# Optimization experiments

Measured on AMD Instinct MI355X. Metric: run time of the kernel, lower is better.

## Reference

```python
import jax, jax.numpy as jnp
import numpy as np


def _lstm_scan(x, mask, W_ih, W_hh, h0, c0):
    # x: [B,S,D], mask: [B,S] bool. Masked LSTM (bias=False, PyTorch gate order i,f,g,o).
    def step(carry, inp):
        h, c = carry
        xt, mt = inp
        gates = xt @ W_ih.T + h @ W_hh.T          # [B, 4H]
        i, f, g, o = jnp.split(gates, 4, axis=-1)
        c_new = jax.nn.sigmoid(f) * c + jax.nn.sigmoid(i) * jnp.tanh(g)
        h_new = jax.nn.sigmoid(o) * jnp.tanh(c_new)
        m = mt[:, None]
        h = jnp.where(m, h_new, h)
        c = jnp.where(m, c_new, c)
        return (h, c), h
    (hT, cT), hs = jax.lax.scan(step, (h0, c0), (x.swapaxes(0, 1), mask.T))
    return hs.swapaxes(0, 1), hT, cT  # [B,S,H], [B,H], [B,H]


def setup_inputs() -> dict:
    key = jax.random.key(0)
    ks = jax.random.split(key, 24)
    B, S, V, E, H, DA, R, MH = 64, 1024, 50000, 300, 256, 64, 16, 512
    N_ET, N_PRT, N_POPT = 50, 12, 8
    sc = 1.0 / np.sqrt(H)
    input_ids = jax.random.randint(ks[0], (B, S), 0, V)
    len_li = jnp.sort(jax.random.randint(ks[1], (B,), S // 2, S + 1))[::-1]  # descending, >=1
    inp = {
        'input_ids': input_ids,
        'len_li': len_li,
        'h0': jnp.zeros((2, B, H), jnp.float32),
        'c0': jnp.zeros((2, B, H), jnp.float32),
        'emb': jax.random.normal(ks[2], (V, E), jnp.float32) * 0.1,
        'W_ih_f': jax.random.normal(ks[3], (4 * H, E), jnp.float32) * sc,
        'W_hh_f': jax.random.normal(ks[4], (4 * H, H), jnp.float32) * sc,
        'W_ih_b': jax.random.normal(ks[5], (4 * H, E), jnp.float32) * sc,
        'W_hh_b': jax.random.normal(ks[6], (4 * H, H), jnp.float32) * sc,
        'S1': jax.random.uniform(ks[7], (DA, 2 * H), jnp.float32, -0.1, 0.1),
        'S2': jax.random.uniform(ks[8], (R, DA), jnp.float32, -0.1, 0.1),
        'W_et': jax.random.uniform(ks[9], (MH, R * 2 * H), jnp.float32, -0.1, 0.1),
        'b_et': jnp.zeros((MH,), jnp.float32),
        'Wd_et': jax.random.uniform(ks[10], (N_ET, MH), jnp.float32, -0.1, 0.1),
        'bd_et': jnp.zeros((N_ET,), jnp.float32),
        'W_prt': jax.random.uniform(ks[11], (MH, R * 2 * H), jnp.float32, -0.1, 0.1),
        'b_prt': jnp.zeros((MH,), jnp.float32),
        'Wd_prt': jax.random.uniform(ks[12], (N_PRT, MH), jnp.float32, -0.1, 0.1),
        'bd_prt': jnp.zeros((N_PRT,), jnp.float32),
        'W_popt': jax.random.uniform(ks[13], (MH, R * 2 * H), jnp.float32, -0.1, 0.1),
        'b_popt': jnp.zeros((MH,), jnp.float32),
        'Wd_popt': jax.random.uniform(ks[14], (N_POPT, MH), jnp.float32, -0.1, 0.1),
        'bd_popt': jnp.zeros((N_POPT,), jnp.float32),
    }
    return inp


def reference(input_ids, len_li, h0, c0, emb, W_ih_f, W_hh_f, W_ih_b, W_hh_b,
              S1, S2, W_et, b_et, Wd_et, bd_et, W_prt, b_prt, Wd_prt, bd_prt,
              W_popt, b_popt, Wd_popt, bd_popt):
    B, S = input_ids.shape
    t = jnp.arange(S)[None, :]
    mask = t < len_li[:, None]                                  # [B,S]
    x = emb[input_ids]                                          # [B,S,E]
    # forward direction
    out_f, hf, cf = _lstm_scan(x, mask, W_ih_f, W_hh_f, h0[0], c0[0])
    # backward direction: reverse each sequence within its own length (involution)
    rev_idx = jnp.clip(len_li[:, None] - 1 - t, 0, S - 1)       # [B,S]
    x_rev = jnp.take_along_axis(x, rev_idx[:, :, None], axis=1)
    out_b_rev, hb, cb = _lstm_scan(x_rev, mask, W_ih_b, W_hh_b, h0[1], c0[1])
    out_b = jnp.take_along_axis(out_b_rev, rev_idx[:, :, None], axis=1)
    Hout = jnp.concatenate([out_f, out_b], axis=-1)             # [B,S,2H]
    # self-attention: A = softmax over valid positions, per row of r
    s2 = jnp.tanh(Hout @ S1.T) @ S2.T                           # [B,S,r]
    NEG = jnp.asarray(-1e30, Hout.dtype)
    scores = jnp.where(mask[:, :, None], s2, NEG).swapaxes(1, 2)  # [B,r,S]
    A = jax.nn.softmax(scores, axis=-1)                         # [B,r,S]
    M = jnp.einsum('brs,bsd->brd', A, Hout)                     # [B,r,2H]
    BM = M.reshape(B, -1)                                       # [B, r*2H]
    AAT = jnp.einsum('brs,bqs->brq', A, A)                      # [B,r,r]
    I = jnp.eye(A.shape[1], dtype=A.dtype)
    penal = jnp.mean(jnp.sum((AAT - I) ** 2, axis=(1, 2)))      # mean ||AA^T - I||_F^2
    def head(W, b, Wd, bd):
        return jax.nn.relu(BM @ W.T + b) @ Wd.T + bd
    decoded_et = head(W_et, b_et, Wd_et, bd_et)
    decoded_prt = head(W_prt, b_prt, Wd_prt, bd_prt)
    decoded_popt = head(W_popt, b_popt, Wd_popt, bd_popt)
    hidden = (jnp.stack([hf, hb]), jnp.stack([cf, cb]))
    return (decoded_et, decoded_prt, decoded_popt, hidden, penal, A)
```

## Files before the change

kernel.cpp:

```cpp
#include <hip/hip_runtime.h>
#include <cstdint>
#include <cstddef>

typedef short bf16x8 __attribute__((ext_vector_type(8)));
typedef float f32x4 __attribute__((ext_vector_type(4)));

#define DEVI static __device__ __forceinline__

DEVI unsigned short f2bf(float f) {
  union { float f; unsigned u; } v; v.f = f;
  unsigned r = (v.u + 0x7fffu + ((v.u >> 16) & 1u)) >> 16;
  return (unsigned short)r;
}
DEVI float bf2f(unsigned short s) {
  union { unsigned u; float f; } v; v.u = ((unsigned)s) << 16;
  return v.f;
}
DEVI float sigf(float x) { return 1.f / (1.f + __expf(-x)); }
DEVI float tanh_f(float x) {
  float xc = fminf(fmaxf(x, -15.f), 15.f);
  float e = __expf(2.f * xc);
  return 1.f - 2.f / (e + 1.f);
}
DEVI unsigned long long ldg_sc1_64(const unsigned long long* p) {
  return __hip_atomic_load(p, __ATOMIC_RELAXED, __HIP_MEMORY_SCOPE_AGENT);
}
DEVI void stg_sc1(unsigned* p, unsigned v) {
  __hip_atomic_store(p, v, __ATOMIC_RELAXED, __HIP_MEMORY_SCOPE_AGENT);
}

#define DO_ET     0
#define DO_PRT    3200
#define DO_POPT   3968
#define DO_H      4480
#define DO_C      37248
#define DO_PENAL  70016
#define DO_A      70017

__global__ __launch_bounds__(256) void k_pack(
    const float* __restrict__ Wih_f, const float* __restrict__ Wih_b,
    const float* __restrict__ Whh_f, const float* __restrict__ Whh_b,
    const float* __restrict__ S1,
    unsigned short* __restrict__ BihP, unsigned short* __restrict__ BhhP,
    unsigned short* __restrict__ S1P, int* __restrict__ flags, float* __restrict__ dout)
{
  int idx = blockIdx.x * 256 + threadIdx.x;
  if (idx < 655360) {
    int d = idx / 327680; int e = idx % 327680;
    int kb = e / 8192; int rem = e % 8192; int n = rem >> 3; int j = rem & 7;
    int k = kb * 8 + j;
    int col = ((n >> 5) & 3) * 256 + ((n >> 7) << 5) + (n & 31);
    const float* W = d ? Wih_b : Wih_f;
    float v = (k < 300) ? W[col * 300 + k] : 0.f;
    BihP[idx] = f2bf(v);
  } else if (idx < 1179648) {
    int e = idx - 655360;
    int d = e >> 18; int e2 = e & 262143;
    int ht = (e2 >> 15) & 7; int kb = (e2 >> 10) & 31; int c = (e2 >> 3) & 127; int j = e2 & 7;
    int k = kb * 8 + j;
    int row = ((c >> 5) << 8) + (ht << 5) + (c & 31);
    const float* W = d ? Whh_b : Whh_f;
    BhhP[e] = f2bf(W[row * 256 + k]);
  } else if (idx < 1212416) {
    int e = idx - 1179648;
    int j = e & 7; int da = (e >> 3) & 63; int kb = e >> 9;
    S1P[e] = f2bf(S1[da * 512 + kb * 8 + j]);
  } else if (idx < 1213440) {
    flags[idx - 1212416] = 0;
  } else if (idx == 1213440) {
    dout[DO_PENAL] = 0.f;
  }
}

__global__ __launch_bounds__(256, 1) void k_rnn(
    const int* __restrict__ ids, const float* __restrict__ emb,
    const unsigned short* __restrict__ BihP, const unsigned short* __restrict__ BhhP,
    unsigned short* __restrict__ Hbuf, unsigned short* __restrict__ Hout, int* flags,
    const int* __restrict__ len, const float* __restrict__ h0, const float* __restrict__ c0,
    float* __restrict__ dout)
{
  int blk = blockIdx.x;
  int ht = blk >> 3; int g = blk & 7; int d = g >> 2; int bt = g & 3;
  int tid = threadIdx.x;
  int lane = tid & 63, w = tid >> 6, l15 = lane & 15, quad = lane >> 4;
  int b0 = bt * 16;

  __shared__ unsigned short Wl[40960];
  __shared__ unsigned short Xl[2][5120];
  __shared__ unsigned short h0p[4096];
  __shared__ float gatesL[2048];
  __shared__ int lenS[16];

  {
    const unsigned* src = (const unsigned*)(BihP + (size_t)d * 327680);
    unsigned* dstW = (unsigned*)Wl;
    for (int kb = 0; kb < 40; ++kb) {
      int gb = ((kb * 1024 + ht * 128) * 8) >> 1;
      for (int i = tid; i < 512; i += 256)
        dstW[kb * 512 + i] = src[gb + i];
    }
  }
  for (int i = tid; i < 4096; i += 256) {
    int kb = i >> 7, mm = (i >> 3) & 15, j = i & 7;
    h0p[i] = f2bf(h0[d * 16384 + (b0 + mm) * 256 + kb * 8 + j]);
  }
  if (tid < 16) lenS[tid] = len[b0 + tid];
  for (int i = tid; i < 128; i += 256) {
    ((unsigned*)Xl[0])[2432 + i] = 0;
    ((unsigned*)Xl[1])[2432 + i] = 0;
  }
  const unsigned short* Bw = BhhP + (size_t)(d * 8 + ht) * 32768;
  bf16x8 bfr[8][2];
  #pragma unroll
  for (int kc = 0; kc < 8; ++kc)
    #pragma unroll
    for (int nt = 0; nt < 2; ++nt)
      bfr[kc][nt] = *reinterpret_cast<const bf16x8*>(
          Bw + ((size_t)(kc * 4 + quad) * 128 + w * 32 + nt * 16 + l15) * 8);

  __syncthreads();

  int xm = tid >> 4, xf = tid & 15;
  {
    int lbm = lenS[xm];
    int s = d ? (lbm - 1) : 0;
    s = s < 0 ? 0 : (s > 1023 ? 1023 : s);
    int tok = ids[(b0 + xm) * 1024 + s];
    const float* er = emb + (size_t)tok * 300;
    #pragma unroll
    for (int i = 0; i < 5; ++i) {
      int f = xf + 16 * i;
      float4 v = (f <= 74) ? *reinterpret_cast<const float4*>(er + 4 * f)
                           : (float4){0.f, 0.f, 0.f, 0.f};
      if (f < 76) {
        int uo = ((f >> 1) * 16 + xm) * 4 + (f & 1) * 2;
        ((unsigned*)Xl[0])[uo]     = (unsigned)f2bf(v.x) | ((unsigned)f2bf(v.y) << 16);
        ((unsigned*)Xl[0])[uo + 1] = (unsigned)f2bf(v.z) | ((unsigned)f2bf(v.w) << 16);
      }
    }
  }
  __syncthreads();

  int b_l = tid >> 4, u2 = tid & 15;
  int len_b = lenS[b_l];
  int Tmax = lenS[0];
  int cidx = d * 16384 + (b0 + b_l) * 256 + ht * 32 + 2 * u2;
  float cc0 = c0[cidx], cc1 = c0[cidx + 1];
  float hh0 = h0[cidx], hh1 = h0[cidx + 1];

  unsigned short* HbufG = Hbuf + (size_t)g * 8192;
  int* fl = flags + g * 128;

  for (int t = 0; t < Tmax; ++t) {
    float4 xr[5];
    {
      int tn = t + 1;
      int s = d ? (lenS[xm] - 1 - tn) : tn;
      s = s < 0 ? 0 : (s > 1023 ? 1023 : s);
      int tok = ids[(b0 + xm) * 1024 + s];
      const float* er = emb + (size_t)tok * 300;
      #pragma unroll
      for (int i = 0; i < 5; ++i) {
        int f = xf + 16 * i;
        xr[i] = (f <= 74) ? *reinterpret_cast<const float4*>(er + 4 * f)
                          : (float4){0.f, 0.f, 0.f, 0.f};
      }
    }

    f32x4 ac0 = {0.f, 0.f, 0.f, 0.f}, ac1 = {0.f, 0.f, 0.f, 0.f};
    {
      const unsigned short* Xb = Xl[t & 1];
      #pragma unroll
      for (int kc = 0; kc < 10; ++kc) {
        int kb = kc * 4 + quad;
        bf16x8 ax  = *reinterpret_cast<const bf16x8*>(&Xb[(kb * 16 + l15) * 8]);
        bf16x8 bx0 = *reinterpret_cast<const bf16x8*>(&Wl[kb * 1024 + (w * 32 + l15) * 8]);
        bf16x8 bx1 = *reinterpret_cast<const bf16x8*>(&Wl[kb * 1024 + (w * 32 + 16 + l15) * 8]);
        ac0 = __builtin_amdgcn_mfma_f32_16x16x32_bf16(ax, bx0, ac0, 0, 0, 0);
        ac1 = __builtin_amdgcn_mfma_f32_16x16x32_bf16(ax, bx1, ac1, 0, 0, 0);
      }
    }

    bf16x8 ah[8];
    if (t == 0) {
      #pragma unroll
      for (int kc = 0; kc < 8; ++kc)
        ah[kc] = *reinterpret_cast<const bf16x8*>(&h0p[((kc * 4 + quad) * 16 + l15) * 8]);
    } else {
      int polls = 0;
      while (true) {
        int v = 0x7fffffff;
        if (lane < 8)
          v = __hip_atomic_load(fl + lane * 16, __ATOMIC_RELAXED, __HIP_MEMORY_SCOPE_AGENT);
        if (__ballot(v >= t) == ~0ull) break;
        if (++polls > 100000) break;
      }
      asm volatile("" ::: "memory");
      const unsigned long long* slotU =
          (const unsigned long long*)(HbufG + (size_t)(t & 1) * 4096);
      #pragma unroll
      for (int kc = 0; kc < 8; ++kc) {
        int qo = (((kc * 4 + quad) * 16 + l15) * 4) >> 1;
        union { unsigned long long q[2]; bf16x8 v; } tu;
        tu.q[0] = ldg_sc1_64(slotU + qo);
        tu.q[1] = ldg_sc1_64(slotU + qo + 1);
        ah[kc] = tu.v;
      }
    }
    #pragma unroll
    for (int kc = 0; kc < 8; ++kc) {
      ac0 = __builtin_amdgcn_mfma_f32_16x16x32_bf16(ah[kc], bfr[kc][0], ac0, 0, 0, 0);
      ac1 = __builtin_amdgcn_mfma_f32_16x16x32_bf16(ah[kc], bfr[kc][1], ac1, 0, 0, 0);
    }

    #pragma unroll
    for (int r = 0; r < 4; ++r) {
      gatesL[(w * 16 + quad * 4 + r) * 32 + l15] = ac0[r];
      gatesL[(w * 16 + quad * 4 + r) * 32 + 16 + l15] = ac1[r];
    }
    __syncthreads();

    float gi0 = gatesL[(0 * 16 + b_l) * 32 + 2 * u2], gi1 = gatesL[(0 * 16 + b_l) * 32 + 2 * u2 + 1];
    float gf0 = gatesL[(1 * 16 + b_l) * 32 + 2 * u2], gf1 = gatesL[(1 * 16 + b_l) * 32 + 2 * u2 + 1];
    float gg0 = gatesL[(2 * 16 + b_l) * 32 + 2 * u2], gg1 = gatesL[(2 * 16 + b_l) * 32 + 2 * u2 + 1];
    float go0 = gatesL[(3 * 16 + b_l) * 32 + 2 * u2], go1 = gatesL[(3 * 16 + b_l) * 32 + 2 * u2 + 1];

    if (t < len_b) {
      float cn0 = sigf(gf0) * cc0 + sigf(gi0) * tanh_f(gg0);
      float cn1 = sigf(gf1) * cc1 + sigf(gi1) * tanh_f(gg1);
      cc0 = cn0; cc1 = cn1;
      hh0 = sigf(go0) * tanh_f(cn0);
      hh1 = sigf(go1) * tanh_f(cn1);
    }

    int k = ht * 32 + 2 * u2;
    unsigned hp = (unsigned)f2bf(hh0) | ((unsigned)f2bf(hh1) << 16);
    unsigned soff = ((unsigned)(k >> 3) * 128 + b_l * 8 + (k & 7)) >> 1;
    stg_sc1((unsigned*)(HbufG + (size_t)((t + 1) & 1) * 4096) + soff, hp);

    {
      unsigned* LX = (unsigned*)Xl[(t + 1) & 1];
      #pragma unroll
      for (int i = 0; i < 5; ++i) {
        int f = xf + 16 * i;
        if (f < 76) {
          int uo = ((f >> 1) * 16 + xm) * 4 + (f & 1) * 2;
          LX[uo]     = (unsigned)f2bf(xr[i].x) | ((unsigned)f2bf(xr[i].y) << 16);
          LX[uo + 1] = (unsigned)f2bf(xr[i].z) | ((unsigned)f2bf(xr[i].w) << 16);
        }
      }
    }

    __syncthreads();
    if (tid == 0)
      __hip_atomic_store(fl + ht * 16, t + 1, __ATOMIC_RELAXED, __HIP_MEMORY_SCOPE_AGENT);

    size_t hob = (size_t)(b0 + b_l) * 524288;
    if (d == 0) {
      *reinterpret_cast<unsigned*>(Hout + hob + (size_t)t * 512 + k) = hp;
    } else if (t < len_b) {
      *reinterpret_cast<unsigned*>(Hout + hob + (size_t)(len_b - 1 - t) * 512 + 256 + k) = hp;
    }
    if (t == len_b - 1) {
      dout[DO_H + cidx] = hh0; dout[DO_H + cidx + 1] = hh1;
      dout[DO_C + cidx] = cc0; dout[DO_C + cidx + 1] = cc1;
    }
  }
}

__global__ __launch_bounds__(256, 2) void k_scores(
    const unsigned short* __restrict__ Hout, const unsigned short* __restrict__ S1P,
    const float* __restrict__ S2, float* __restrict__ scores)
{
  __shared__ float U[128 * 65];
  __shared__ float S2l[16 * 65];
  int tid = threadIdx.x;
  int t0 = blockIdx.x * 128;
  int b = blockIdx.y;
  int lane = tid & 63, w = tid >> 6, l15 = lane & 15, quad = lane >> 4;

  f32x4 acc[2][4];
  #pragma unroll
  for (int i = 0; i < 2; ++i)
    #pragma unroll
    for (int j = 0; j < 4; ++j) acc[i][j] = (f32x4){0.f, 0.f, 0.f, 0.f};

  for (int kc = 0; kc < 16; ++kc) {
    bf16x8 afr[2];
    #pragma unroll
    for (int mt = 0; mt < 2; ++mt) {
      int row = t0 + w * 32 + mt * 16 + l15;
      afr[mt] = *reinterpret_cast<const bf16x8*>(
          Hout + (size_t)b * 524288 + (size_t)row * 512 + kc * 32 + quad * 8);
    }
    bf16x8 bfr[4];
    #pragma unroll
    for (int nt = 0; nt < 4; ++nt)
      bfr[nt] = *reinterpret_cast<const bf16x8*>(
          S1P + ((size_t)(kc * 4 + quad) * 64 + nt * 16 + l15) * 8);
    #pragma unroll
    for (int mt = 0; mt < 2; ++mt)
      #pragma unroll
      for (int nt = 0; nt < 4; ++nt)
        acc[mt][nt] = __builtin_amdgcn_mfma_f32_16x16x32_bf16(afr[mt], bfr[nt], acc[mt][nt], 0, 0, 0);
  }
  #pragma unroll
  for (int mt = 0; mt < 2; ++mt)
    #pragma unroll
    for (int nt = 0; nt < 4; ++nt)
      #pragma unroll
      for (int r = 0; r < 4; ++r)
        U[(w * 32 + mt * 16 + quad * 4 + r) * 65 + nt * 16 + l15] = acc[mt][nt][r];
  for (int i = tid; i < 1024; i += 256) S2l[(i >> 6) * 65 + (i & 63)] = S2[i];
  __syncthreads();
  for (int i = tid; i < 8192; i += 256) {
    int row = i >> 6, c = i & 63;
    U[row * 65 + c] = tanh_f(U[row * 65 + c]);
  }
  __syncthreads();
  for (int idx = tid; idx < 2048; idx += 256) {
    int row = idx >> 4, r = idx & 15;
    float s = 0.f;
    #pragma unroll 8
    for (int da = 0; da < 64; ++da) s += U[row * 65 + da] * S2l[r * 65 + da];
    scores[((size_t)b * 16 + r) * 1024 + t0 + row] = s;
  }
}

__global__ __launch_bounds__(256) void k_softmax(
    const float* __restrict__ scores, const int* __restrict__ len, float* __restrict__ dout)
{
  __shared__ float red[256];
  int b = blockIdx.x, r = blockIdx.y;
  int tid = threadIdx.x;
  int lb = len[b];
  const float* src = scores + ((size_t)b * 16 + r) * 1024;
  float v[4]; float mx = -3.0e38f;
  #pragma unroll
  for (int i = 0; i < 4; ++i) {
    int t = tid + i * 256;
    v[i] = (t < lb) ? src[t] : -3.0e38f;
    mx = fmaxf(mx, v[i]);
  }
  red[tid] = mx; __syncthreads();
  for (int s = 128; s > 0; s >>= 1) { if (tid < s) red[tid] = fmaxf(red[tid], red[tid + s]); __syncthreads(); }
  float M = red[0]; __syncthreads();
  float se = 0.f;
  #pragma unroll
  for (int i = 0; i < 4; ++i) {
    int t = tid + i * 256;
    if (t < lb) { v[i] = __expf(v[i] - M); se += v[i]; }
  }
  red[tid] = se; __syncthreads();
  for (int s = 128; s > 0; s >>= 1) { if (tid < s) red[tid] += red[tid + s]; __syncthreads(); }
  float inv = 1.f / red[0];
  float* dst = dout + DO_A + ((size_t)b * 16 + r) * 1024;
  #pragma unroll
  for (int i = 0; i < 4; ++i) {
    int t = tid + i * 256;
    dst[t] = (t < lb) ? v[i] * inv : 0.f;
  }
}

__global__ __launch_bounds__(256) void k_penal(float* __restrict__ dout)
{
  __shared__ float Al[16 * 513];
  __shared__ float red[256];
  int b = blockIdx.x, tid = threadIdx.x;
  const float* A = dout + DO_A + (size_t)b * 16384;
  int r = tid >> 4, q = tid & 15;
  float s = 0.f;
  for (int half = 0; half < 2; ++half) {
    __syncthreads();
    for (int i = tid; i < 8192; i += 256) {
      int rr = i >> 9, t = i & 511;
      Al[rr * 513 + t] = A[rr * 1024 + half * 512 + t];
    }
    __syncthreads();
    for (int t = 0; t < 512; ++t) s += Al[r * 513 + t] * Al[q * 513 + t];
  }
  float dv = s - ((r == q) ? 1.f : 0.f);
  red[tid] = dv * dv; __syncthreads();
  for (int st = 128; st > 0; st >>= 1) { if (tid < st) red[tid] += red[tid + st]; __syncthreads(); }
  if (tid == 0) atomicAdd(dout + DO_PENAL, red[0] * (1.f / 64.f));
}

__global__ __launch_bounds__(256) void k_attnM(
    const float* __restrict__ dout, const unsigned short* __restrict__ Hout,
    const int* __restrict__ len, float* __restrict__ Mws)
{
  int b = blockIdx.x, dc = blockIdx.y;
  int tid = threadIdx.x;
  int col = dc * 128 + (tid & 127);
  int rh = tid >> 7;
  int lb = len[b];
  const float* Ab = dout + DO_A + (size_t)b * 16384;
  const unsigned short* Hb = Hout + (size_t)b * 524288;
  float acc[8];
  #pragma unroll
  for (int i = 0; i < 8; ++i) acc[i] = 0.f;
  for (int t = 0; t < lb; ++t) {
    float h = bf2f(Hb[(size_t)t * 512 + col]);
    #pragma unroll
    for (int rr = 0; rr < 8; ++rr) acc[rr] += Ab[(rh * 8 + rr) * 1024 + t] * h;
  }
  #pragma unroll
  for (int rr = 0; rr < 8; ++rr) Mws[(size_t)b * 8192 + (rh * 8 + rr) * 512 + col] = acc[rr];
}

__global__ __launch_bounds__(256) void k_heads1(
    const float* __restrict__ W, const float* __restrict__ Mws, float* __restrict__ P)
{
  int tid = threadIdx.x;
  int n = blockIdx.x * 16 + (tid & 15);
  int ks = blockIdx.y;
  int bg = tid >> 4;
  const float* Wr = W + (size_t)n * 8192 + ks * 1024;
  float acc[4] = {0.f, 0.f, 0.f, 0.f};
  for (int k = 0; k < 1024; k += 4) {
    float4 wv = *reinterpret_cast<const float4*>(Wr + k);
    #pragma unroll
    for (int i = 0; i < 4; ++i) {
      float4 mv = *reinterpret_cast<const float4*>(Mws + (size_t)(bg * 4 + i) * 8192 + ks * 1024 + k);
      acc[i] += wv.x * mv.x + wv.y * mv.y + wv.z * mv.z + wv.w * mv.w;
    }
  }
  #pragma unroll
  for (int i = 0; i < 4; ++i)
    P[(size_t)(ks * 64 + bg * 4 + i) * 512 + n] = acc[i];
}

__global__ __launch_bounds__(256) void k_headred(
    const float* __restrict__ Pws, const float* __restrict__ b_et,
    const float* __restrict__ b_prt, const float* __restrict__ b_popt,
    float* __restrict__ hid)
{
  int idx = blockIdx.x * 256 + threadIdx.x;
  int head = idx >> 15; int rem = idx & 32767;
  int b = rem >> 9; int n = rem & 511;
  const float* bias = (head == 0) ? b_et : (head == 1) ? b_prt : b_popt;
  float s = bias[n];
  #pragma unroll
  for (int ks = 0; ks < 8; ++ks)
    s += Pws[(size_t)(head * 8 + ks) * 32768 + b * 512 + n];
  hid[idx] = fmaxf(s, 0.f);
}

__global__ __launch_bounds__(256) void k_head2(
    const float* __restrict__ hid, const float* __restrict__ Wd, const float* __restrict__ bd,
    float* __restrict__ out, int No)
{
  int idx = blockIdx.x * 256 + threadIdx.x;
  if (idx >= 64 * No) return;
  int b = idx / No, o = idx % No;
  const float* hv = hid + (size_t)b * 512;
  const float* wr = Wd + (size_t)o * 512;
  float acc = bd[o];
  for (int k = 0; k < 512; k += 4) {
    float4 h4 = *reinterpret_cast<const float4*>(hv + k);
    float4 w4 = *reinterpret_cast<const float4*>(wr + k);
    acc += h4.x * w4.x + h4.y * w4.y + h4.z * w4.z + h4.w * w4.w;
  }
  out[idx] = acc;
}

extern "C" void kernel_launch(void* const* d_in, const int* in_sizes, int n_in,
                              void* d_out, int out_size, void* d_ws, size_t ws_size,
                              hipStream_t stream) {
  const int*   ids    = (const int*)d_in[0];
  const int*   len    = (const int*)d_in[1];
  const float* h0     = (const float*)d_in[2];
  const float* c0     = (const float*)d_in[3];
  const float* emb    = (const float*)d_in[4];
  const float* Wih_f  = (const float*)d_in[5];
  const float* Whh_f  = (const float*)d_in[6];
  const float* Wih_b  = (const float*)d_in[7];
  const float* Whh_b  = (const float*)d_in[8];
  const float* S1     = (const float*)d_in[9];
  const float* S2     = (const float*)d_in[10];
  const float* W_et   = (const float*)d_in[11];
  const float* b_et   = (const float*)d_in[12];
  const float* Wd_et  = (const float*)d_in[13];
  const float* bd_et  = (const float*)d_in[14];
  const float* W_prt  = (const float*)d_in[15];
  const float* b_prt  = (const float*)d_in[16];
  const float* Wd_prt = (const float*)d_in[17];
  const float* bd_prt = (const float*)d_in[18];
  const float* W_popt = (const float*)d_in[19];
  const float* b_popt = (const float*)d_in[20];
  const float* Wd_popt= (const float*)d_in[21];
  const float* bd_popt= (const float*)d_in[22];
  float* dout = (float*)d_out;
  char* ws = (char*)d_ws;

  size_t off = 0;
  auto AL = [&](size_t bytes) { size_t r = off; off += (bytes + 255) & ~(size_t)255; return r; };
  size_t oHout = AL(67108864UL);
  size_t oBih  = AL(1310720UL);
  size_t oBhh  = AL(1048576UL);
  size_t oS1P  = AL(65536UL);
  size_t oHbuf = AL(131072UL);
  size_t oFlag = AL(4096UL);
  size_t oPws  = AL(3145728UL);
  size_t oSc   = AL(4194304UL);
  size_t oM    = oSc;
  size_t oHid  = oSc + 2097152UL;

  unsigned short* Hout = (unsigned short*)(ws + oHout);
  unsigned short* BihP = (unsigned short*)(ws + oBih);
  unsigned short* BhhP = (unsigned short*)(ws + oBhh);
  unsigned short* S1P  = (unsigned short*)(ws + oS1P);
  unsigned short* Hbuf = (unsigned short*)(ws + oHbuf);
  int* flags           = (int*)(ws + oFlag);
  float* Pws           = (float*)(ws + oPws);
  float* scores        = (float*)(ws + oSc);
  float* Mws           = (float*)(ws + oM);
  float* hid           = (float*)(ws + oHid);

  hipLaunchKernelGGL(k_pack, dim3(4741), dim3(256), 0, stream,
                     Wih_f, Wih_b, Whh_f, Whh_b, S1, BihP, BhhP, S1P, flags, dout);
  hipLaunchKernelGGL(k_rnn, dim3(64), dim3(256), 0, stream,
                     ids, emb, BihP, BhhP, Hbuf, Hout, flags, len, h0, c0, dout);
  hipLaunchKernelGGL(k_scores, dim3(8, 64), dim3(256), 0, stream, Hout, S1P, S2, scores);
  hipLaunchKernelGGL(k_softmax, dim3(64, 16), dim3(256), 0, stream, scores, len, dout);
  hipLaunchKernelGGL(k_penal, dim3(64), dim3(256), 0, stream, dout);
  hipLaunchKernelGGL(k_attnM, dim3(64, 4), dim3(256), 0, stream, dout, Hout, len, Mws);
  hipLaunchKernelGGL(k_heads1, dim3(32, 8), dim3(256), 0, stream, W_et,   Mws, Pws);
  hipLaunchKernelGGL(k_heads1, dim3(32, 8), dim3(256), 0, stream, W_prt,  Mws, Pws + 262144);
  hipLaunchKernelGGL(k_heads1, dim3(32, 8), dim3(256), 0, stream, W_popt, Mws, Pws + 524288);
  hipLaunchKernelGGL(k_headred, dim3(384), dim3(256), 0, stream, Pws, b_et, b_prt, b_popt, hid);
  hipLaunchKernelGGL(k_head2, dim3(13), dim3(256), 0, stream, hid,         Wd_et,   bd_et,   dout + DO_ET, 50);
  hipLaunchKernelGGL(k_head2, dim3(3),  dim3(256), 0, stream, hid + 32768, Wd_prt,  bd_prt,  dout + DO_PRT, 12);
  hipLaunchKernelGGL(k_head2, dim3(2),  dim3(256), 0, stream, hid + 65536, Wd_popt, bd_popt, dout + DO_POPT, 8);
}
```

Baseline: 3.456 ms.

## Keep all LSTM weights in registers and split hidden dim over 4 blocks

```diff
diff --git a/kernel.cpp b/kernel.cpp
--- a/kernel.cpp
+++ b/kernel.cpp
@@ -25,7 +25,7 @@
 DEVI unsigned long long ldg_sc1_64(const unsigned long long* p) {
   return __hip_atomic_load(p, __ATOMIC_RELAXED, __HIP_MEMORY_SCOPE_AGENT);
 }
-DEVI void stg_sc1(unsigned* p, unsigned v) {
+DEVI void stg_sc1_64(unsigned long long* p, unsigned long long v) {
   __hip_atomic_store(p, v, __ATOMIC_RELAXED, __HIP_MEMORY_SCOPE_AGENT);
 }
 
@@ -46,21 +46,29 @@
 {
   int idx = blockIdx.x * 256 + threadIdx.x;
   if (idx < 655360) {
-    int d = idx / 327680; int e = idx % 327680;
-    int kb = e / 8192; int rem = e % 8192; int n = rem >> 3; int j = rem & 7;
-    int k = kb * 8 + j;
-    int col = ((n >> 5) & 3) * 256 + ((n >> 7) << 5) + (n & 31);
+    int dq = idx / 81920; int e = idx % 81920;
+    int d = dq >> 2; int q = dq & 3;
+    int j = e & 7; int lane = (e >> 3) & 63;
+    int r1 = e >> 9;
+    int kc = r1 % 10; int wg = r1 / 10;
+    int gg = wg & 3; int w = wg >> 2;
+    int l15 = lane & 15, quad = lane >> 4;
+    int row = gg * 256 + q * 64 + w * 16 + l15;
+    int k = kc * 32 + quad * 8 + j;
     const float* W = d ? Wih_b : Wih_f;
-    float v = (k < 300) ? W[col * 300 + k] : 0.f;
+    float v = (k < 300) ? W[row * 300 + k] : 0.f;
     BihP[idx] = f2bf(v);
   } else if (idx < 1179648) {
-    int e = idx - 655360;
-    int d = e >> 18; int e2 = e & 262143;
-    int ht = (e2 >> 15) & 7; int kb = (e2 >> 10) & 31; int c = (e2 >> 3) & 127; int j = e2 & 7;
-    int k = kb * 8 + j;
-    int row = ((c >> 5) << 8) + (ht << 5) + (c & 31);
+    int e0 = idx - 655360;
+    int dq = e0 >> 16; int e = e0 & 65535;
+    int d = dq >> 2; int q = dq & 3;
+    int j = e & 7; int lane = (e >> 3) & 63;
+    int kc = (e >> 9) & 7; int gg = (e >> 12) & 3; int w = e >> 14;
+    int l15 = lane & 15, quad = lane >> 4;
+    int row = gg * 256 + q * 64 + w * 16 + l15;
+    int k = kc * 32 + quad * 8 + j;
     const float* W = d ? Whh_b : Whh_f;
-    BhhP[e] = f2bf(W[row * 256 + k]);
+    BhhP[e0] = f2bf(W[row * 256 + k]);
   } else if (idx < 1212416) {
     int e = idx - 1179648;
     int j = e & 7; int da = (e >> 3) & 63; int kb = e >> 9;
@@ -80,26 +88,32 @@
     float* __restrict__ dout)
 {
   int blk = blockIdx.x;
-  int ht = blk >> 3; int g = blk & 7; int d = g >> 2; int bt = g & 3;
+  int q = blk >> 3;
+  int g = blk & 7; int d = g >> 2; int bt = g & 3;
   int tid = threadIdx.x;
   int lane = tid & 63, w = tid >> 6, l15 = lane & 15, quad = lane >> 4;
   int b0 = bt * 16;
 
-  __shared__ unsigned short Wl[40960];
   __shared__ unsigned short Xl[2][5120];
   __shared__ unsigned short h0p[4096];
-  __shared__ float gatesL[2048];
   __shared__ int lenS[16];
 
-  {
-    const unsigned* src = (const unsigned*)(BihP + (size_t)d * 327680);
-    unsigned* dstW = (unsigned*)Wl;
-    for (int kb = 0; kb < 40; ++kb) {
-      int gb = ((kb * 1024 + ht * 128) * 8) >> 1;
-      for (int i = tid; i < 512; i += 256)
-        dstW[kb * 512 + i] = src[gb + i];
-    }
-  }
+  const unsigned short* BA = BihP + (size_t)(d * 4 + q) * 81920;
+  const unsigned short* BH = BhhP + (size_t)(d * 4 + q) * 65536;
+  bf16x8 wih[4][10];
+  bf16x8 whh[4][8];
+  #pragma unroll
+  for (int gg = 0; gg < 4; ++gg) {
+    #pragma unroll
+    for (int kc = 0; kc < 10; ++kc)
+      wih[gg][kc] = *reinterpret_cast<const bf16x8*>(
+          BA + ((size_t)(((w * 4 + gg) * 10 + kc) * 64 + lane)) * 8);
+    #pragma unroll
+    for (int kc = 0; kc < 8; ++kc)
+      whh[gg][kc] = *reinterpret_cast<const bf16x8*>(
+          BH + ((size_t)(((w * 4 + gg) * 8 + kc) * 64 + lane)) * 8);
+  }
+
   for (int i = tid; i < 4096; i += 256) {
     int kb = i >> 7, mm = (i >> 3) & 15, j = i & 7;
     h0p[i] = f2bf(h0[d * 16384 + (b0 + mm) * 256 + kb * 8 + j]);
@@ -109,21 +123,12 @@
     ((unsigned*)Xl[0])[2432 + i] = 0;
     ((unsigned*)Xl[1])[2432 + i] = 0;
   }
-  const unsigned short* Bw = BhhP + (size_t)(d * 8 + ht) * 32768;
-  bf16x8 bfr[8][2];
-  #pragma unroll
-  for (int kc = 0; kc < 8; ++kc)
-    #pragma unroll
-    for (int nt = 0; nt < 2; ++nt)
-      bfr[kc][nt] = *reinterpret_cast<const bf16x8*>(
-          Bw + ((size_t)(kc * 4 + quad) * 128 + w * 32 + nt * 16 + l15) * 8);
-
   __syncthreads();
 
   int xm = tid >> 4, xf = tid & 15;
+  int len_xm = lenS[xm];
   {
-    int lbm = lenS[xm];
-    int s = d ? (lbm - 1) : 0;
+    int s = d ? (len_xm - 1) : 0;
     s = s < 0 ? 0 : (s > 1023 ? 1023 : s);
     int tok = ids[(b0 + xm) * 1024 + s];
     const float* er = emb + (size_t)tok * 300;
@@ -141,21 +146,28 @@
   }
   __syncthreads();
 
-  int b_l = tid >> 4, u2 = tid & 15;
-  int len_b = lenS[b_l];
+  int len_my = lenS[l15];
   int Tmax = lenS[0];
-  int cidx = d * 16384 + (b0 + b_l) * 256 + ht * 32 + 2 * u2;
-  float cc0 = c0[cidx], cc1 = c0[cidx + 1];
-  float hh0 = h0[cidx], hh1 = h0[cidx + 1];
+  int dimb = q * 64 + w * 16 + quad * 4;
+  int cidx = d * 16384 + (b0 + l15) * 256 + dimb;
+  float cc[4], hh[4];
+  {
+    float4 c4 = *reinterpret_cast<const float4*>(c0 + cidx);
+    float4 h4 = *reinterpret_cast<const float4*>(h0 + cidx);
+    cc[0] = c4.x; cc[1] = c4.y; cc[2] = c4.z; cc[3] = c4.w;
+    hh[0] = h4.x; hh[1] = h4.y; hh[2] = h4.z; hh[3] = h4.w;
+  }
 
   unsigned short* HbufG = Hbuf + (size_t)g * 8192;
   int* fl = flags + g * 128;
+  int slotKB = dimb >> 3;
+  int slotJ  = dimb & 7;
 
   for (int t = 0; t < Tmax; ++t) {
     float4 xr[5];
     {
       int tn = t + 1;
-      int s = d ? (lenS[xm] - 1 - tn) : tn;
+      int s = d ? (len_xm - 1 - tn) : tn;
       s = s < 0 ? 0 : (s > 1023 ? 1023 : s);
       int tok = ids[(b0 + xm) * 1024 + s];
       const float* er = emb + (size_t)tok * 300;
@@ -167,17 +179,17 @@
       }
     }
 
-    f32x4 ac0 = {0.f, 0.f, 0.f, 0.f}, ac1 = {0.f, 0.f, 0.f, 0.f};
+    f32x4 acc0 = {0.f, 0.f, 0.f, 0.f};
+    f32x4 acc1 = acc0, acc2 = acc0, acc3 = acc0;
     {
       const unsigned short* Xb = Xl[t & 1];
       #pragma unroll
       for (int kc = 0; kc < 10; ++kc) {
-        int kb = kc * 4 + quad;
-        bf16x8 ax  = *reinterpret_cast<const bf16x8*>(&Xb[(kb * 16 + l15) * 8]);
-        bf16x8 bx0 = *reinterpret_cast<const bf16x8*>(&Wl[kb * 1024 + (w * 32 + l15) * 8]);
-        bf16x8 bx1 = *reinterpret_cast<const bf16x8*>(&Wl[kb * 1024 + (w * 32 + 16 + l15) * 8]);
-        ac0 = __builtin_amdgcn_mfma_f32_16x16x32_bf16(ax, bx0, ac0, 0, 0, 0);
-        ac1 = __builtin_amdgcn_mfma_f32_16x16x32_bf16(ax, bx1, ac1, 0, 0, 0);
+        bf16x8 bx = *reinterpret_cast<const bf16x8*>(&Xb[((kc * 4 + quad) * 16 + l15) * 8]);
+        acc0 = __builtin_amdgcn_mfma_f32_16x16x32_bf16(wih[0][kc], bx, acc0, 0, 0, 0);
+        acc1 = __builtin_amdgcn_mfma_f32_16x16x32_bf16(wih[1][kc], bx, acc1, 0, 0, 0);
+        acc2 = __builtin_amdgcn_mfma_f32_16x16x32_bf16(wih[2][kc], bx, acc2, 0, 0, 0);
+        acc3 = __builtin_amdgcn_mfma_f32_16x16x32_bf16(wih[3][kc], bx, acc3, 0, 0, 0);
       }
     }
 
@@ -190,7 +202,7 @@
       int polls = 0;
       while (true) {
         int v = 0x7fffffff;
-        if (lane < 8)
+        if (lane < 4)
           v = __hip_atomic_load(fl + lane * 16, __ATOMIC_RELAXED, __HIP_MEMORY_SCOPE_AGENT);
         if (__ballot(v >= t) == ~0ull) break;
         if (++polls > 100000) break;
@@ -200,43 +212,52 @@
           (const unsigned long long*)(HbufG + (size_t)(t & 1) * 4096);
       #pragma unroll
       for (int kc = 0; kc < 8; ++kc) {
-        int qo = (((kc * 4 + quad) * 16 + l15) * 4) >> 1;
-        union { unsigned long long q[2]; bf16x8 v; } tu;
-        tu.q[0] = ldg_sc1_64(slotU + qo);
-        tu.q[1] = ldg_sc1_64(slotU + qo + 1);
+        int qo = ((kc * 4 + quad) * 16 + l15) * 2;
+        union { unsigned long long u[2]; bf16x8 v; } tu;
+        tu.u[0] = ldg_sc1_64(slotU + qo);
+        tu.u[1] = ldg_sc1_64(slotU + qo + 1);
         ah[kc] = tu.v;
       }
     }
     #pragma unroll
     for (int kc = 0; kc < 8; ++kc) {
-      ac0 = __builtin_amdgcn_mfma_f32_16x16x32_bf16(ah[kc], bfr[kc][0], ac0, 0, 0, 0);
-      ac1 = __builtin_amdgcn_mfma_f32_16x16x32_bf16(ah[kc], bfr[kc][1], ac1, 0, 0, 0);
-    }
-
-    #pragma unroll
-    for (int r = 0; r < 4; ++r) {
-      gatesL[(w * 16 + quad * 4 + r) * 32 + l15] = ac0[r];
-      gatesL[(w * 16 + quad * 4 + r) * 32 + 16 + l15] = ac1[r];
-    }
-    __syncthreads();
-
-    float gi0 = gatesL[(0 * 16 + b_l) * 32 + 2 * u2], gi1 = gatesL[(0 * 16 + b_l) * 32 + 2 * u2 + 1];
-    float gf0 = gatesL[(1 * 16 + b_l) * 32 + 2 * u2], gf1 = gatesL[(1 * 16 + b_l) * 32 + 2 * u2 + 1];
-    float gg0 = gatesL[(2 * 16 + b_l) * 32 + 2 * u2], gg1 = gatesL[(2 * 16 + b_l) * 32 + 2 * u2 + 1];
-    float go0 = gatesL[(3 * 16 + b_l) * 32 + 2 * u2], go1 = gatesL[(3 * 16 + b_l) * 32 + 2 * u2 + 1];
-
-    if (t < len_b) {
-      float cn0 = sigf(gf0) * cc0 + sigf(gi0) * tanh_f(gg0);
-      float cn1 = sigf(gf1) * cc1 + sigf(gi1) * tanh_f(gg1);
-      cc0 = cn0; cc1 = cn1;
-      hh0 = sigf(go0) * tanh_f(cn0);
-      hh1 = sigf(go1) * tanh_f(cn1);
-    }
-
-    int k = ht * 32 + 2 * u2;
-    unsigned hp = (unsigned)f2bf(hh0) | ((unsigned)f2bf(hh1) << 16);
-    unsigned soff = ((unsigned)(k >> 3) * 128 + b_l * 8 + (k & 7)) >> 1;
-    stg_sc1((unsigned*)(HbufG + (size_t)((t + 1) & 1) * 4096) + soff, hp);
+      acc0 = __builtin_amdgcn_mfma_f32_16x16x32_bf16(whh[0][kc], ah[kc], acc0, 0, 0, 0);
+      acc1 = __builtin_amdgcn_mfma_f32_16x16x32_bf16(whh[1][kc], ah[kc], acc1, 0, 0, 0);
+      acc2 = __builtin_amdgcn_mfma_f32_16x16x32_bf16(whh[2][kc], ah[kc], acc2, 0, 0, 0);
+      acc3 = __builtin_amdgcn_mfma_f32_16x16x32_bf16(whh[3][kc], ah[kc], acc3, 0, 0, 0);
+    }
+
+    if (t < len_my) {
+      #pragma unroll
+      for (int r = 0; r < 4; ++r) {
+        float cn = sigf(acc1[r]) * cc[r] + sigf(acc0[r]) * tanh_f(acc2[r]);
+        cc[r] = cn;
+        hh[r] = sigf(acc3[r]) * tanh_f(cn);
+      }
+    }
+
+    union { unsigned long long u; unsigned short s[4]; } hp;
+    #pragma unroll
+    for (int r = 0; r < 4; ++r) hp.s[r] = f2bf(hh[r]);
+
+    stg_sc1_64((unsigned long long*)(HbufG + (size_t)((t + 1) & 1) * 4096)
+                   + ((slotKB * 128 + l15 * 8 + slotJ) >> 2),
+               hp.u);
+    asm volatile("s_waitcnt vmcnt(0)" ::: "memory");
+    __builtin_amdgcn_s_barrier();
+    if (tid == 0)
+      __hip_atomic_store(fl + q * 16, t + 1, __ATOMIC_RELAXED, __HIP_MEMORY_SCOPE_AGENT);
+
+    size_t hob = (size_t)(b0 + l15) * 524288 + (size_t)d * 256 + dimb;
+    if (d == 0) {
+      *reinterpret_cast<unsigned long long*>(Hout + hob + (size_t)t * 512) = hp.u;
+    } else if (t < len_my) {
+      *reinterpret_cast<unsigned long long*>(Hout + hob + (size_t)(len_my - 1 - t) * 512) = hp.u;
+    }
+    if (t == len_my - 1) {
+      *reinterpret_cast<float4*>(dout + DO_H + cidx) = (float4){hh[0], hh[1], hh[2], hh[3]};
+      *reinterpret_cast<float4*>(dout + DO_C + cidx) = (float4){cc[0], cc[1], cc[2], cc[3]};
+    }
 
     {
       unsigned* LX = (unsigned*)Xl[(t + 1) & 1];
@@ -250,21 +271,7 @@
         }
       }
     }
-
     __syncthreads();
-    if (tid == 0)
-      __hip_atomic_store(fl + ht * 16, t + 1, __ATOMIC_RELAXED, __HIP_MEMORY_SCOPE_AGENT);
-
-    size_t hob = (size_t)(b0 + b_l) * 524288;
-    if (d == 0) {
-      *reinterpret_cast<unsigned*>(Hout + hob + (size_t)t * 512 + k) = hp;
-    } else if (t < len_b) {
-      *reinterpret_cast<unsigned*>(Hout + hob + (size_t)(len_b - 1 - t) * 512 + 256 + k) = hp;
-    }
-    if (t == len_b - 1) {
-      dout[DO_H + cidx] = hh0; dout[DO_H + cidx + 1] = hh1;
-      dout[DO_C + cidx] = cc0; dout[DO_C + cidx + 1] = cc1;
-    }
   }
 }
 
@@ -519,7 +526,7 @@
 
   hipLaunchKernelGGL(k_pack, dim3(4741), dim3(256), 0, stream,
                      Wih_f, Wih_b, Whh_f, Whh_b, S1, BihP, BhhP, S1P, flags, dout);
-  hipLaunchKernelGGL(k_rnn, dim3(64), dim3(256), 0, stream,
+  hipLaunchKernelGGL(k_rnn, dim3(32), dim3(256), 0, stream,
                      ids, emb, BihP, BhhP, Hbuf, Hout, flags, len, h0, c0, dout);
   hipLaunchKernelGGL(k_scores, dim3(8, 64), dim3(256), 0, stream, Hout, S1P, S2, scores);
   hipLaunchKernelGGL(k_softmax, dim3(64, 16), dim3(256), 0, stream, scores, len, dout);
```

Result: slower. 4.016 ms (+16.2%).

## Swap MFMA operands so gates land in registers, drop LDS gate exchange

Applied to the files above, without the earlier changes.

```diff
diff --git a/kernel.cpp b/kernel.cpp
--- a/kernel.cpp
+++ b/kernel.cpp
@@ -47,20 +47,29 @@
   int idx = blockIdx.x * 256 + threadIdx.x;
   if (idx < 655360) {
     int d = idx / 327680; int e = idx % 327680;
-    int kb = e / 8192; int rem = e % 8192; int n = rem >> 3; int j = rem & 7;
-    int k = kb * 8 + j;
-    int col = ((n >> 5) & 3) * 256 + ((n >> 7) << 5) + (n & 31);
+    int j = e & 7; int lane = (e >> 3) & 63;
+    int r1 = e >> 9;
+    int kc = r1 % 10; int r2 = r1 / 10;
+    int mt = r2 & 1; int w = (r2 >> 1) & 3; int ht = r2 >> 3;
+    int l15 = lane & 15, quad = lane >> 4;
+    int gate = l15 & 3, dimoff = l15 >> 2;
+    int dim = ht * 32 + w * 8 + 2 * dimoff + mt;
+    int row = gate * 256 + dim;
+    int k = kc * 32 + quad * 8 + j;
     const float* W = d ? Wih_b : Wih_f;
-    float v = (k < 300) ? W[col * 300 + k] : 0.f;
-    BihP[idx] = f2bf(v);
+    BihP[idx] = f2bf((k < 300) ? W[row * 300 + k] : 0.f);
   } else if (idx < 1179648) {
-    int e = idx - 655360;
-    int d = e >> 18; int e2 = e & 262143;
-    int ht = (e2 >> 15) & 7; int kb = (e2 >> 10) & 31; int c = (e2 >> 3) & 127; int j = e2 & 7;
-    int k = kb * 8 + j;
-    int row = ((c >> 5) << 8) + (ht << 5) + (c & 31);
+    int e0 = idx - 655360;
+    int d = e0 >> 18; int e = e0 & 262143;
+    int j = e & 7; int lane = (e >> 3) & 63;
+    int kc = (e >> 9) & 7; int mt = (e >> 12) & 1; int w = (e >> 13) & 3; int ht = (e >> 15) & 7;
+    int l15 = lane & 15, quad = lane >> 4;
+    int gate = l15 & 3, dimoff = l15 >> 2;
+    int dim = ht * 32 + w * 8 + 2 * dimoff + mt;
+    int row = gate * 256 + dim;
+    int k = kc * 32 + quad * 8 + j;
     const float* W = d ? Whh_b : Whh_f;
-    BhhP[e] = f2bf(W[row * 256 + k]);
+    BhhP[e0] = f2bf(W[row * 256 + k]);
   } else if (idx < 1212416) {
     int e = idx - 1179648;
     int j = e & 7; int da = (e >> 3) & 63; int kb = e >> 9;
@@ -85,21 +94,27 @@
   int lane = tid & 63, w = tid >> 6, l15 = lane & 15, quad = lane >> 4;
   int b0 = bt * 16;
 
-  __shared__ unsigned short Wl[40960];
   __shared__ unsigned short Xl[2][5120];
   __shared__ unsigned short h0p[4096];
-  __shared__ float gatesL[2048];
   __shared__ int lenS[16];
 
-  {
-    const unsigned* src = (const unsigned*)(BihP + (size_t)d * 327680);
-    unsigned* dstW = (unsigned*)Wl;
-    for (int kb = 0; kb < 40; ++kb) {
-      int gb = ((kb * 1024 + ht * 128) * 8) >> 1;
-      for (int i = tid; i < 512; i += 256)
-        dstW[kb * 512 + i] = src[gb + i];
-    }
-  }
+  const unsigned short* BA = BihP + (size_t)d * 327680;
+  const unsigned short* BH = BhhP + (size_t)d * 262144;
+  int hw = ht * 4 + w;
+  bf16x8 wih[2][10];
+  bf16x8 whh[2][8];
+  #pragma unroll
+  for (int mt = 0; mt < 2; ++mt) {
+    #pragma unroll
+    for (int kc = 0; kc < 10; ++kc)
+      wih[mt][kc] = *reinterpret_cast<const bf16x8*>(
+          BA + ((size_t)(((hw * 2 + mt) * 10 + kc) * 64 + lane)) * 8);
+    #pragma unroll
+    for (int kc = 0; kc < 8; ++kc)
+      whh[mt][kc] = *reinterpret_cast<const bf16x8*>(
+          BH + ((size_t)(((hw * 2 + mt) * 8 + kc) * 64 + lane)) * 8);
+  }
+
   for (int i = tid; i < 4096; i += 256) {
     int kb = i >> 7, mm = (i >> 3) & 15, j = i & 7;
     h0p[i] = f2bf(h0[d * 16384 + (b0 + mm) * 256 + kb * 8 + j]);
@@ -109,15 +124,6 @@
     ((unsigned*)Xl[0])[2432 + i] = 0;
     ((unsigned*)Xl[1])[2432 + i] = 0;
   }
-  const unsigned short* Bw = BhhP + (size_t)(d * 8 + ht) * 32768;
-  bf16x8 bfr[8][2];
-  #pragma unroll
-  for (int kc = 0; kc < 8; ++kc)
-    #pragma unroll
-    for (int nt = 0; nt < 2; ++nt)
-      bfr[kc][nt] = *reinterpret_cast<const bf16x8*>(
-          Bw + ((size_t)(kc * 4 + quad) * 128 + w * 32 + nt * 16 + l15) * 8);
-
   __syncthreads();
 
   int xm = tid >> 4, xf = tid & 15;
@@ -141,10 +147,10 @@
   }
   __syncthreads();
 
-  int b_l = tid >> 4, u2 = tid & 15;
-  int len_b = lenS[b_l];
+  int len_my = lenS[l15];
   int Tmax = lenS[0];
-  int cidx = d * 16384 + (b0 + b_l) * 256 + ht * 32 + 2 * u2;
+  int k0 = ht * 32 + w * 8 + 2 * quad;
+  int cidx = d * 16384 + (b0 + l15) * 256 + k0;
   float cc0 = c0[cidx], cc1 = c0[cidx + 1];
   float hh0 = h0[cidx], hh1 = h0[cidx + 1];
 
@@ -167,17 +173,14 @@
       }
     }
 
-    f32x4 ac0 = {0.f, 0.f, 0.f, 0.f}, ac1 = {0.f, 0.f, 0.f, 0.f};
+    f32x4 a0 = {0.f, 0.f, 0.f, 0.f}, a1 = {0.f, 0.f, 0.f, 0.f};
     {
       const unsigned short* Xb = Xl[t & 1];
       #pragma unroll
       for (int kc = 0; kc < 10; ++kc) {
-        int kb = kc * 4 + quad;
-        bf16x8 ax  = *reinterpret_cast<const bf16x8*>(&Xb[(kb * 16 + l15) * 8]);
-        bf16x8 bx0 = *reinterpret_cast<const bf16x8*>(&Wl[kb * 1024 + (w * 32 + l15) * 8]);
-        bf16x8 bx1 = *reinterpret_cast<const bf16x8*>(&Wl[kb * 1024 + (w * 32 + 16 + l15) * 8]);
-        ac0 = __builtin_amdgcn_mfma_f32_16x16x32_bf16(ax, bx0, ac0, 0, 0, 0);
-        ac1 = __builtin_amdgcn_mfma_f32_16x16x32_bf16(ax, bx1, ac1, 0, 0, 0);
+        bf16x8 bx = *reinterpret_cast<const bf16x8*>(&Xb[((kc * 4 + quad) * 16 + l15) * 8]);
+        a0 = __builtin_amdgcn_mfma_f32_16x16x32_bf16(wih[0][kc], bx, a0, 0, 0, 0);
+        a1 = __builtin_amdgcn_mfma_f32_16x16x32_bf16(wih[1][kc], bx, a1, 0, 0, 0);
       }
     }
 
@@ -209,34 +212,19 @@
     }
     #pragma unroll
     for (int kc = 0; kc < 8; ++kc) {
-      ac0 = __builtin_amdgcn_mfma_f32_16x16x32_bf16(ah[kc], bfr[kc][0], ac0, 0, 0, 0);
-      ac1 = __builtin_amdgcn_mfma_f32_16x16x32_bf16(ah[kc], bfr[kc][1], ac1, 0, 0, 0);
-    }
-
-    #pragma unroll
-    for (int r = 0; r < 4; ++r) {
-      gatesL[(w * 16 + quad * 4 + r) * 32 + l15] = ac0[r];
-      gatesL[(w * 16 + quad * 4 + r) * 32 + 16 + l15] = ac1[r];
-    }
-    __syncthreads();
-
-    float gi0 = gatesL[(0 * 16 + b_l) * 32 + 2 * u2], gi1 = gatesL[(0 * 16 + b_l) * 32 + 2 * u2 + 1];
-    float gf0 = gatesL[(1 * 16 + b_l) * 32 + 2 * u2], gf1 = gatesL[(1 * 16 + b_l) * 32 + 2 * u2 + 1];
-    float gg0 = gatesL[(2 * 16 + b_l) * 32 + 2 * u2], gg1 = gatesL[(2 * 16 + b_l) * 32 + 2 * u2 + 1];
-    float go0 = gatesL[(3 * 16 + b_l) * 32 + 2 * u2], go1 = gatesL[(3 * 16 + b_l) * 32 + 2 * u2 + 1];
-
-    if (t < len_b) {
-      float cn0 = sigf(gf0) * cc0 + sigf(gi0) * tanh_f(gg0);
-      float cn1 = sigf(gf1) * cc1 + sigf(gi1) * tanh_f(gg1);
-      cc0 = cn0; cc1 = cn1;
-      hh0 = sigf(go0) * tanh_f(cn0);
-      hh1 = sigf(go1) * tanh_f(cn1);
-    }
-
-    int k = ht * 32 + 2 * u2;
+      a0 = __builtin_amdgcn_mfma_f32_16x16x32_bf16(whh[0][kc], ah[kc], a0, 0, 0, 0);
+      a1 = __builtin_amdgcn_mfma_f32_16x16x32_bf16(whh[1][kc], ah[kc], a1, 0, 0, 0);
+    }
+
+    if (t < len_my) {
+      float cn0 = sigf(a0[1]) * cc0 + sigf(a0[0]) * tanh_f(a0[2]);
+      cc0 = cn0; hh0 = sigf(a0[3]) * tanh_f(cn0);
+      float cn1 = sigf(a1[1]) * cc1 + sigf(a1[0]) * tanh_f(a1[2]);
+      cc1 = cn1; hh1 = sigf(a1[3]) * tanh_f(cn1);
+    }
+
     unsigned hp = (unsigned)f2bf(hh0) | ((unsigned)f2bf(hh1) << 16);
-    unsigned soff = ((unsigned)(k >> 3) * 128 + b_l * 8 + (k & 7)) >> 1;
-    stg_sc1((unsigned*)(HbufG + (size_t)((t + 1) & 1) * 4096) + soff, hp);
+    stg_sc1((unsigned*)(HbufG + (size_t)((t + 1) & 1) * 4096) + (hw * 64 + l15 * 4 + quad), hp);
 
     {
       unsigned* LX = (unsigned*)Xl[(t + 1) & 1];
@@ -255,13 +243,13 @@
     if (tid == 0)
       __hip_atomic_store(fl + ht * 16, t + 1, __ATOMIC_RELAXED, __HIP_MEMORY_SCOPE_AGENT);
 
-    size_t hob = (size_t)(b0 + b_l) * 524288;
+    size_t hob = (size_t)(b0 + l15) * 524288;
     if (d == 0) {
-      *reinterpret_cast<unsigned*>(Hout + hob + (size_t)t * 512 + k) = hp;
-    } else if (t < len_b) {
-      *reinterpret_cast<unsigned*>(Hout + hob + (size_t)(len_b - 1 - t) * 512 + 256 + k) = hp;
-    }
-    if (t == len_b - 1) {
+      *reinterpret_cast<unsigned*>(Hout + hob + (size_t)t * 512 + k0) = hp;
+    } else if (t < len_my) {
+      *reinterpret_cast<unsigned*>(Hout + hob + (size_t)(len_my - 1 - t) * 512 + 256 + k0) = hp;
+    }
+    if (t == len_my - 1) {
       dout[DO_H + cidx] = hh0; dout[DO_H + cidx + 1] = hh1;
       dout[DO_C + cidx] = cc0; dout[DO_C + cidx + 1] = cc1;
     }
```

Measured after the change: 3.287 ms. -4.9%, faster.
